# Kernel tuning notes

Measured on AMD Instinct MI355X. Metric: run time of the kernel, lower is better.

The kernel has to match this reference:

```python
import jax, jax.numpy as jnp
import numpy as np

NUM_EXPERT = 16
IN_FEAT = 1024
OUT_FEAT = 2048
N_TOKENS = 4096


def setup_inputs() -> dict:
    key = jax.random.key(0)
    k1, k2, k3 = jax.random.split(key, 3)
    x = jax.random.uniform(k1, (N_TOKENS, IN_FEAT), dtype=jnp.float32)
    gate = jax.random.randint(k2, (N_TOKENS,), 0, NUM_EXPERT, dtype=jnp.int32)
    # expert weights: [num_expert, out_feat, in_feat]
    weight = jax.random.normal(k3, (NUM_EXPERT, OUT_FEAT, IN_FEAT), dtype=jnp.float32) * 0.02
    return {"x": x, "gate": gate, "weight": weight}


def reference(x, gate, weight):
    # out[b] = weight[gate[b]] @ x[b]
    # Avoid materializing weight[gate] ([B, O, I] would be huge): scan over the
    # small, fixed expert axis with input masking (tokens not routed to expert e
    # contribute zero rows to that expert's GEMM).
    B = x.shape[0]
    E, O, I = weight.shape
    out0 = jnp.zeros((B, O), dtype=x.dtype)

    def body(out, ew):
        e, W = ew  # W: [O, I]
        xm = jnp.where((gate == e)[:, None], x, 0.0)  # [B, I] masked tokens
        return out + jnp.einsum("bi,oi->bo", xm, W), None

    out, _ = jax.lax.scan(body, out0, (jnp.arange(E), weight))
    return out
```

## Files before the change

kernel.cpp:

```cpp
#include <hip/hip_runtime.h>
#include <hip/hip_bf16.h>
#include <stdint.h>

#define N_TOKENS   4096
#define IN_FEAT    1024
#define OUT_FEAT   2048
#define NUM_EXPERT 16

#define BM 128
#define BN 128
#define BK 32
#define NT (IN_FEAT / BK)
#define MAX_TILES 48
#define MAX_ROWS  6144

typedef __bf16 bf16x8 __attribute__((ext_vector_type(8)));
typedef float  f32x4  __attribute__((ext_vector_type(4)));
typedef unsigned short us8 __attribute__((ext_vector_type(8)));

__device__ __forceinline__ unsigned short f32_to_bf16_rne(float f) {
  union { float f; uint32_t u; } v; v.f = f;
  uint32_t u = v.u;
  u += 0x7fffu + ((u >> 16) & 1u);
  return (unsigned short)(u >> 16);
}

__device__ __forceinline__ void async_copy16(const void* g, void* l) {
  __builtin_amdgcn_global_load_lds(
      (const __attribute__((address_space(1))) unsigned int*)g,
      (__attribute__((address_space(3))) unsigned int*)l, 16, 0, 0);
}

__global__ void k_setup(const int* __restrict__ gate,
                        int* __restrict__ pstart,
                        int* __restrict__ tile_e,
                        int* __restrict__ tile_m,
                        int* __restrict__ row_token)
{
  __shared__ int cnt[NUM_EXPERT];
  __shared__ int cur[NUM_EXPERT];
  __shared__ int ps[NUM_EXPERT];
  const int tid = threadIdx.x;
  if (tid < NUM_EXPERT) { cnt[tid] = 0; cur[tid] = 0; }
  __syncthreads();
  for (int b = tid; b < N_TOKENS; b += 256) atomicAdd(&cnt[gate[b]], 1);
  for (int r = tid; r < MAX_ROWS; r += 256) row_token[r] = -1;
  __syncthreads();
  if (tid == 0) {
    int p = 0, tot = 0;
    for (int e = 0; e < NUM_EXPERT; ++e) {
      ps[e] = p; pstart[e] = p;
      int nt = (cnt[e] + BM - 1) / BM;
      for (int t = 0; t < nt; ++t) { tile_e[tot] = e; tile_m[tot] = t; ++tot; }
      p += nt * BM;
    }
    for (int s = tot; s < MAX_TILES; ++s) { tile_e[s] = -1; tile_m[s] = 0; }
  }
  __syncthreads();
  for (int b = tid; b < N_TOKENS; b += 256) {
    int e = gate[b];
    int pos = atomicAdd(&cur[e], 1);
    row_token[ps[e] + pos] = b;
  }
}

__global__ void k_gather_x(const float4* __restrict__ x,
                           const int* __restrict__ row_token,
                           us8* __restrict__ xs) {
  const int r = blockIdx.x * 2 + (threadIdx.x >> 7);
  const int c = threadIdx.x & 127;
  const int tok = row_token[r];
  us8 o;
  if (tok >= 0) {
    float4 a = x[tok * 256 + c * 2];
    float4 b = x[tok * 256 + c * 2 + 1];
    o[0] = f32_to_bf16_rne(a.x); o[1] = f32_to_bf16_rne(a.y);
    o[2] = f32_to_bf16_rne(a.z); o[3] = f32_to_bf16_rne(a.w);
    o[4] = f32_to_bf16_rne(b.x); o[5] = f32_to_bf16_rne(b.y);
    o[6] = f32_to_bf16_rne(b.z); o[7] = f32_to_bf16_rne(b.w);
  } else {
    o = (us8)0;
  }
  xs[r * 128 + c] = o;
}

__global__ void __launch_bounds__(256)
k_gemm(const unsigned short* __restrict__ xs,
       const float* __restrict__ w,
       const int* __restrict__ pstart,
       const int* __restrict__ tile_e,
       const int* __restrict__ tile_m,
       const int* __restrict__ row_token,
       float* __restrict__ out) {
  __shared__ us8   As[2][512];
  __shared__ f32x4 Bs[2][1024];
  __shared__ int rowtok_s[BM];

  const int slot = blockIdx.y;
  const int e = tile_e[slot];
  if (e < 0) return;
  const int seg0 = pstart[e] + tile_m[slot] * BM;
  const int n0 = blockIdx.x * BN;

  const int tid  = threadIdx.x;
  const int wid  = tid >> 6;
  const int lane = tid & 63;
  const int lr   = lane & 15;
  const int quad = lane >> 4;
  const int wm   = (wid >> 1) * 64;
  const int wn   = (wid & 1) * 64;

  if (tid < BM) rowtok_s[tid] = row_token[seg0 + tid];

  const int cA = (tid & 3) ^ ((tid >> 3) & 3);
  const int cB = (tid & 7) ^ ((tid >> 3) & 7);
  const unsigned short* agp = xs + (size_t)(seg0 + (tid >> 2)) * IN_FEAT + cA * 8;
  const float* bgp = w + (size_t)e * OUT_FEAT * IN_FEAT
                       + (size_t)(n0 + (tid >> 3)) * IN_FEAT + cB * 4;

  f32x4 acc[4][4];
  const f32x4 z = {0.f, 0.f, 0.f, 0.f};
#pragma unroll
  for (int i = 0; i < 4; ++i)
#pragma unroll
    for (int j = 0; j < 4; ++j) acc[i][j] = z;

  auto stage = [&](int t, int b) {
    const int k0 = t * BK;
    async_copy16(agp + k0,                 As[b] + wid * 64);
    async_copy16(agp + 64 * IN_FEAT + k0,  As[b] + 256 + wid * 64);
    async_copy16(bgp + k0,                 Bs[b] + wid * 64);
    async_copy16(bgp + 32 * IN_FEAT + k0,  Bs[b] + 256 + wid * 64);
    async_copy16(bgp + 64 * IN_FEAT + k0,  Bs[b] + 512 + wid * 64);
    async_copy16(bgp + 96 * IN_FEAT + k0,  Bs[b] + 768 + wid * 64);
  };

  stage(0, 0);

  asm volatile("s_waitcnt lgkmcnt(0)" ::: "memory");
  __builtin_amdgcn_s_barrier();

  for (int t = 0; t < NT; ++t) {
    const int buf = t & 1;
    if (t + 1 < NT) {
      stage(t + 1, buf ^ 1);
      asm volatile("s_waitcnt vmcnt(6)" ::: "memory");
    } else {
      asm volatile("s_waitcnt vmcnt(0)" ::: "memory");
    }
    __builtin_amdgcn_s_barrier();
    asm volatile("" ::: "memory");

    bf16x8 af[4], bf[4];
#pragma unroll
    for (int mi = 0; mi < 4; ++mi) {
      const int n = wm + mi * 16 + lr;
      af[mi] = *(const bf16x8*)&As[buf][n * 4 + (quad ^ ((n >> 1) & 3))];
    }
#pragma unroll
    for (int ni = 0; ni < 4; ++ni) {
      const int n = wn + ni * 16 + lr;
      f32x4 c0 = Bs[buf][n * 8 + ((2 * quad)     ^ (n & 7))];
      f32x4 c1 = Bs[buf][n * 8 + ((2 * quad + 1) ^ (n & 7))];
      bf16x8 b;
      b[0] = (__bf16)c0[0]; b[1] = (__bf16)c0[1];
      b[2] = (__bf16)c0[2]; b[3] = (__bf16)c0[3];
      b[4] = (__bf16)c1[0]; b[5] = (__bf16)c1[1];
      b[6] = (__bf16)c1[2]; b[7] = (__bf16)c1[3];
      bf[ni] = b;
    }
#pragma unroll
    for (int mi = 0; mi < 4; ++mi)
#pragma unroll
      for (int ni = 0; ni < 4; ++ni)
        acc[mi][ni] = __builtin_amdgcn_mfma_f32_16x16x32_bf16(
            af[mi], bf[ni], acc[mi][ni], 0, 0, 0);

    asm volatile("" ::: "memory");
    __builtin_amdgcn_s_barrier();
  }

#pragma unroll
  for (int mi = 0; mi < 4; ++mi) {
    const int mb = wm + mi * 16 + quad * 4;
    const int t0 = rowtok_s[mb + 0];
    const int t1 = rowtok_s[mb + 1];
    const int t2 = rowtok_s[mb + 2];
    const int t3 = rowtok_s[mb + 3];
#pragma unroll
    for (int ni = 0; ni < 4; ++ni) {
      const int n = n0 + wn + ni * 16 + lr;
      f32x4 c = acc[mi][ni];
      if (t0 >= 0) out[(size_t)t0 * OUT_FEAT + n] = c[0];
      if (t1 >= 0) out[(size_t)t1 * OUT_FEAT + n] = c[1];
      if (t2 >= 0) out[(size_t)t2 * OUT_FEAT + n] = c[2];
      if (t3 >= 0) out[(size_t)t3 * OUT_FEAT + n] = c[3];
    }
  }
}

extern "C" void kernel_launch(void* const* d_in, const int* in_sizes, int n_in,
                              void* d_out, int out_size, void* d_ws, size_t ws_size,
                              hipStream_t stream) {
  const float* x    = (const float*)d_in[0];
  const int*   gate = (const int*)d_in[1];
  const float* w    = (const float*)d_in[2];
  float* out = (float*)d_out;

  char* ws = (char*)d_ws;
  unsigned short* xs = (unsigned short*)ws;
  int* row_token = (int*)(ws + 12582912);
  int* pstart = row_token + MAX_ROWS;
  int* tile_e = pstart + NUM_EXPERT;
  int* tile_m = tile_e + MAX_TILES;

  k_setup<<<1, 256, 0, stream>>>(gate, pstart, tile_e, tile_m, row_token);
  k_gather_x<<<MAX_ROWS / 2, 256, 0, stream>>>((const float4*)x, row_token,
                                               (us8*)xs);
  dim3 g(OUT_FEAT / BN, MAX_TILES);
  k_gemm<<<g, 256, 0, stream>>>(xs, w, pstart, tile_e, tile_m, row_token, out);
}
```

Measured before the change: 260.3 us.

## Load A fragments directly to registers and remap tile order for cache reuse

A fragments are now read from global memory straight into registers, double-buffered across an unrolled pair of k-steps, so the As LDS buffer and its staging disappear. Only the fp32 weight tiles still go through LDS. Block IDs are remapped so that neighbouring blocks share the same expert slots and column tiles, which should improve L2 reuse. Launch bounds now request 3 blocks per CU. The risks are uncoalesced direct global reads of A (16-byte rows strided by IN_FEAT) and higher register pressure.

```diff
diff --git a/kernel.cpp b/kernel.cpp
--- a/kernel.cpp
+++ b/kernel.cpp
@@ -84,7 +84,7 @@
   xs[r * 128 + c] = o;
 }
 
-__global__ void __launch_bounds__(256)
+__global__ void __launch_bounds__(256, 3)
 k_gemm(const unsigned short* __restrict__ xs,
        const float* __restrict__ w,
        const int* __restrict__ pstart,
@@ -92,15 +92,22 @@
        const int* __restrict__ tile_m,
        const int* __restrict__ row_token,
        float* __restrict__ out) {
-  __shared__ us8   As[2][512];
   __shared__ f32x4 Bs[2][1024];
   __shared__ int rowtok_s[BM];
 
-  const int slot = blockIdx.y;
+  const int id  = blockIdx.y * 16 + blockIdx.x;
+  const int r_  = id & 7;
+  const int m_  = id >> 3;
+  const int q3  = m_ % 3;
+  const int n_  = m_ / 3;
+  const int sub = n_ & 1;
+  const int xt  = n_ >> 1;
+
+  const int slot = 2 * (r_ + 8 * q3) + sub;
   const int e = tile_e[slot];
   if (e < 0) return;
   const int seg0 = pstart[e] + tile_m[slot] * BM;
-  const int n0 = blockIdx.x * BN;
+  const int n0 = xt * BN;
 
   const int tid  = threadIdx.x;
   const int wid  = tid >> 6;
@@ -112,12 +119,13 @@
 
   if (tid < BM) rowtok_s[tid] = row_token[seg0 + tid];
 
-  const int cA = (tid & 3) ^ ((tid >> 3) & 3);
   const int cB = (tid & 7) ^ ((tid >> 3) & 7);
-  const unsigned short* agp = xs + (size_t)(seg0 + (tid >> 2)) * IN_FEAT + cA * 8;
   const float* bgp = w + (size_t)e * OUT_FEAT * IN_FEAT
                        + (size_t)(n0 + (tid >> 3)) * IN_FEAT + cB * 4;
 
+  const unsigned short* ap =
+      xs + (size_t)(seg0 + wm + lr) * IN_FEAT + quad * 8;
+
   f32x4 acc[4][4];
   const f32x4 z = {0.f, 0.f, 0.f, 0.f};
 #pragma unroll
@@ -125,38 +133,40 @@
 #pragma unroll
     for (int j = 0; j < 4; ++j) acc[i][j] = z;
 
-  auto stage = [&](int t, int b) {
+  auto stageB = [&](int t, int b) {
     const int k0 = t * BK;
-    async_copy16(agp + k0,                 As[b] + wid * 64);
-    async_copy16(agp + 64 * IN_FEAT + k0,  As[b] + 256 + wid * 64);
     async_copy16(bgp + k0,                 Bs[b] + wid * 64);
     async_copy16(bgp + 32 * IN_FEAT + k0,  Bs[b] + 256 + wid * 64);
     async_copy16(bgp + 64 * IN_FEAT + k0,  Bs[b] + 512 + wid * 64);
     async_copy16(bgp + 96 * IN_FEAT + k0,  Bs[b] + 768 + wid * 64);
   };
-
-  stage(0, 0);
+  auto loadA = [&](int t, bf16x8* dst) {
+#pragma unroll
+    for (int mi = 0; mi < 4; ++mi)
+      dst[mi] = *(const bf16x8*)(ap + (size_t)mi * 16 * IN_FEAT + t * BK);
+  };
+
+  bf16x8 afA[4], afB[4];
+
+  stageB(0, 0);
+  loadA(0, afA);
 
   asm volatile("s_waitcnt lgkmcnt(0)" ::: "memory");
   __builtin_amdgcn_s_barrier();
 
-  for (int t = 0; t < NT; ++t) {
+  auto step = [&](int t, bf16x8* afc, bf16x8* afn) {
     const int buf = t & 1;
     if (t + 1 < NT) {
-      stage(t + 1, buf ^ 1);
-      asm volatile("s_waitcnt vmcnt(6)" ::: "memory");
+      stageB(t + 1, buf ^ 1);
+      loadA(t + 1, afn);
+      asm volatile("s_waitcnt vmcnt(8)" ::: "memory");
     } else {
       asm volatile("s_waitcnt vmcnt(0)" ::: "memory");
     }
     __builtin_amdgcn_s_barrier();
     asm volatile("" ::: "memory");
 
-    bf16x8 af[4], bf[4];
-#pragma unroll
-    for (int mi = 0; mi < 4; ++mi) {
-      const int n = wm + mi * 16 + lr;
-      af[mi] = *(const bf16x8*)&As[buf][n * 4 + (quad ^ ((n >> 1) & 3))];
-    }
+    bf16x8 bf[4];
 #pragma unroll
     for (int ni = 0; ni < 4; ++ni) {
       const int n = wn + ni * 16 + lr;
@@ -174,10 +184,15 @@
 #pragma unroll
       for (int ni = 0; ni < 4; ++ni)
         acc[mi][ni] = __builtin_amdgcn_mfma_f32_16x16x32_bf16(
-            af[mi], bf[ni], acc[mi][ni], 0, 0, 0);
+            afc[mi], bf[ni], acc[mi][ni], 0, 0, 0);
 
     asm volatile("" ::: "memory");
     __builtin_amdgcn_s_barrier();
+  };
+
+  for (int t = 0; t < NT; t += 2) {
+    step(t,     afA, afB);
+    step(t + 1, afB, afA);
   }
 
 #pragma unroll
```

New measurement: 274.9 us. 5.6% more time.

## Gather token rows inside GEMM and double M tile to 256 rows

Applied to the files above, without the earlier changes.

Replaces the separate gather-and-cast kernel with a plain dense fp32-to-bf16 cast of x. The GEMM now loads A rows indirectly through row_token, so each thread holds two per-row source pointers; padded rows point at token 0, and their results are masked at store time. The GEMM also grows to 256x128 tiles with 512 threads, so each expert's weight tile is streamed fewer times. The risk is more padding waste per expert, since an expert with slightly over 256 tokens needs a second, mostly empty tile. Fewer blocks in the grid may also hurt occupancy.

```diff
diff --git a/kernel.cpp b/kernel.cpp
--- a/kernel.cpp
+++ b/kernel.cpp
@@ -7,12 +7,12 @@
 #define OUT_FEAT   2048
 #define NUM_EXPERT 16
 
-#define BM 128
+#define BM 256
 #define BN 128
 #define BK 32
 #define NT (IN_FEAT / BK)
-#define MAX_TILES 48
-#define MAX_ROWS  6144
+#define MAX_TILES 32
+#define MAX_ROWS  8192
 
 typedef __bf16 bf16x8 __attribute__((ext_vector_type(8)));
 typedef float  f32x4  __attribute__((ext_vector_type(4)));
@@ -64,27 +64,19 @@
   }
 }
 
-__global__ void k_gather_x(const float4* __restrict__ x,
-                           const int* __restrict__ row_token,
-                           us8* __restrict__ xs) {
-  const int r = blockIdx.x * 2 + (threadIdx.x >> 7);
-  const int c = threadIdx.x & 127;
-  const int tok = row_token[r];
+__global__ void k_cast(const float4* __restrict__ x, us8* __restrict__ xs) {
+  const int i = blockIdx.x * 256 + threadIdx.x;
+  float4 a = x[i * 2];
+  float4 b = x[i * 2 + 1];
   us8 o;
-  if (tok >= 0) {
-    float4 a = x[tok * 256 + c * 2];
-    float4 b = x[tok * 256 + c * 2 + 1];
-    o[0] = f32_to_bf16_rne(a.x); o[1] = f32_to_bf16_rne(a.y);
-    o[2] = f32_to_bf16_rne(a.z); o[3] = f32_to_bf16_rne(a.w);
-    o[4] = f32_to_bf16_rne(b.x); o[5] = f32_to_bf16_rne(b.y);
-    o[6] = f32_to_bf16_rne(b.z); o[7] = f32_to_bf16_rne(b.w);
-  } else {
-    o = (us8)0;
-  }
-  xs[r * 128 + c] = o;
-}
-
-__global__ void __launch_bounds__(256)
+  o[0] = f32_to_bf16_rne(a.x); o[1] = f32_to_bf16_rne(a.y);
+  o[2] = f32_to_bf16_rne(a.z); o[3] = f32_to_bf16_rne(a.w);
+  o[4] = f32_to_bf16_rne(b.x); o[5] = f32_to_bf16_rne(b.y);
+  o[6] = f32_to_bf16_rne(b.z); o[7] = f32_to_bf16_rne(b.w);
+  xs[i] = o;
+}
+
+__global__ void __launch_bounds__(512, 4)
 k_gemm(const unsigned short* __restrict__ xs,
        const float* __restrict__ w,
        const int* __restrict__ pstart,
@@ -92,7 +84,7 @@
        const int* __restrict__ tile_m,
        const int* __restrict__ row_token,
        float* __restrict__ out) {
-  __shared__ us8   As[2][512];
+  __shared__ us8   As[2][1024];
   __shared__ f32x4 Bs[2][1024];
   __shared__ int rowtok_s[BM];
 
@@ -113,8 +105,14 @@
   if (tid < BM) rowtok_s[tid] = row_token[seg0 + tid];
 
   const int cA = (tid & 3) ^ ((tid >> 3) & 3);
+  const int rt0 = row_token[seg0 + (tid >> 2)];
+  const int rt1 = row_token[seg0 + 128 + (tid >> 2)];
+  const unsigned short* agp0 =
+      xs + (size_t)(rt0 < 0 ? 0 : rt0) * IN_FEAT + cA * 8;
+  const unsigned short* agp1 =
+      xs + (size_t)(rt1 < 0 ? 0 : rt1) * IN_FEAT + cA * 8;
+
   const int cB = (tid & 7) ^ ((tid >> 3) & 7);
-  const unsigned short* agp = xs + (size_t)(seg0 + (tid >> 2)) * IN_FEAT + cA * 8;
   const float* bgp = w + (size_t)e * OUT_FEAT * IN_FEAT
                        + (size_t)(n0 + (tid >> 3)) * IN_FEAT + cB * 4;
 
@@ -127,12 +125,10 @@
 
   auto stage = [&](int t, int b) {
     const int k0 = t * BK;
-    async_copy16(agp + k0,                 As[b] + wid * 64);
-    async_copy16(agp + 64 * IN_FEAT + k0,  As[b] + 256 + wid * 64);
-    async_copy16(bgp + k0,                 Bs[b] + wid * 64);
-    async_copy16(bgp + 32 * IN_FEAT + k0,  Bs[b] + 256 + wid * 64);
+    async_copy16(agp0 + k0,                As[b] +       wid * 64);
+    async_copy16(agp1 + k0,                As[b] + 512 + wid * 64);
+    async_copy16(bgp + k0,                 Bs[b] +       wid * 64);
     async_copy16(bgp + 64 * IN_FEAT + k0,  Bs[b] + 512 + wid * 64);
-    async_copy16(bgp + 96 * IN_FEAT + k0,  Bs[b] + 768 + wid * 64);
   };
 
   stage(0, 0);
@@ -144,7 +140,7 @@
     const int buf = t & 1;
     if (t + 1 < NT) {
       stage(t + 1, buf ^ 1);
-      asm volatile("s_waitcnt vmcnt(6)" ::: "memory");
+      asm volatile("s_waitcnt vmcnt(4)" ::: "memory");
     } else {
       asm volatile("s_waitcnt vmcnt(0)" ::: "memory");
     }
@@ -209,14 +205,14 @@
 
   char* ws = (char*)d_ws;
   unsigned short* xs = (unsigned short*)ws;
-  int* row_token = (int*)(ws + 12582912);
+  int* row_token = (int*)(ws + 8388608);
   int* pstart = row_token + MAX_ROWS;
   int* tile_e = pstart + NUM_EXPERT;
   int* tile_m = tile_e + MAX_TILES;
 
   k_setup<<<1, 256, 0, stream>>>(gate, pstart, tile_e, tile_m, row_token);
-  k_gather_x<<<MAX_ROWS / 2, 256, 0, stream>>>((const float4*)x, row_token,
-                                               (us8*)xs);
+  k_cast<<<N_TOKENS * IN_FEAT / (8 * 256), 256, 0, stream>>>(
+      (const float4*)x, (us8*)xs);
   dim3 g(OUT_FEAT / BN, MAX_TILES);
-  k_gemm<<<g, 256, 0, stream>>>(xs, w, pstart, tile_e, tile_m, row_token, out);
-}
+  k_gemm<<<g, 512, 0, stream>>>(xs, w, pstart, tile_e, tile_m, row_token, out);
+}
```

Measured after the change: 264.9 us. No clear change (+1.7%).
